# Kernel tuning notes

Hardware: AMD Instinct MI355X
Metric: run time of the kernel (lower is better)

## Reference

```python
import jax, jax.numpy as jnp
import numpy as np

N = 4096       # num nodes
E = 131072     # num edges (avg degree 32)
IN = 128       # in_channels
H = 256        # hidden_channels
NC = 16        # num_classes
NH = 4         # num_heads
HD = H // NH   # head dim
EPS = 1e-5


def setup_inputs() -> dict:
    key = jax.random.key(0)
    ks = jax.random.split(key, 16)
    p = lambda k, sh, s=0.05: jax.random.normal(k, sh, jnp.float32) * s
    return {
        "x": jax.random.normal(ks[0], (N, IN), jnp.float32),
        "edge_index": jax.random.randint(ks[1], (2, E), 0, N),
        "edge_attr": jax.random.uniform(ks[2], (E,), jnp.float32),
        # GCN layers
        "W_gcn1": p(ks[3], (IN, H)), "b_gcn1": jnp.zeros((H,), jnp.float32),
        "W_gcn2": p(ks[4], (H, H)), "b_gcn2": jnp.zeros((H,), jnp.float32),
        # Transformer encoder layer (post-norm, batch_first)
        "in_proj_w": p(ks[5], (3 * H, H)), "in_proj_b": jnp.zeros((3 * H,), jnp.float32),
        "out_proj_w": p(ks[6], (H, H)), "out_proj_b": jnp.zeros((H,), jnp.float32),
        "ln1_g": jnp.ones((H,), jnp.float32), "ln1_b": jnp.zeros((H,), jnp.float32),
        "ffn_w1": p(ks[7], (H, 4 * H)), "ffn_b1": jnp.zeros((4 * H,), jnp.float32),
        "ffn_w2": p(ks[8], (4 * H, H)), "ffn_b2": jnp.zeros((H,), jnp.float32),
        "ln2_g": jnp.ones((H,), jnp.float32), "ln2_b": jnp.zeros((H,), jnp.float32),
        # classifier head
        "W_cls": p(ks[9], (H, NC)), "b_cls": jnp.zeros((NC,), jnp.float32),
        # semantic decoder
        "W_d1": p(ks[10], (H, 2 * H)), "b_d1": jnp.zeros((2 * H,), jnp.float32),
        "W_d2": p(ks[11], (2 * H, 3)), "b_d2": jnp.zeros((3,), jnp.float32),
    }


def gcn_conv(x, edge_index, edge_weight, W, b):
    """PyG GCNConv: add self-loops, symmetric norm, gather-matmul-scatter."""
    n = x.shape[0]
    src, dst = edge_index[0], edge_index[1]
    loop = jnp.arange(n)
    src_f = jnp.concatenate([src, loop])
    dst_f = jnp.concatenate([dst, loop])
    ew_f = jnp.concatenate([edge_weight, jnp.ones((n,), x.dtype)])
    deg = jax.ops.segment_sum(ew_f, dst_f, num_segments=n)
    dinv = jnp.where(deg > 0, jax.lax.rsqrt(deg), 0.0)
    norm = dinv[src_f] * ew_f * dinv[dst_f]            # [E+N]
    h = x @ W                                          # [N,H]
    out = jax.ops.segment_sum(norm[:, None] * h[src_f], dst_f, num_segments=n)
    return out + b


def layer_norm(x, g, b):
    mu = jnp.mean(x, axis=-1, keepdims=True)
    var = jnp.mean(jnp.square(x - mu), axis=-1, keepdims=True)
    return (x - mu) * jax.lax.rsqrt(var + EPS) * g + b


def transformer_layer(x, in_proj_w, in_proj_b, out_proj_w, out_proj_b,
                      ln1_g, ln1_b, ffn_w1, ffn_b1, ffn_w2, ffn_b2, ln2_g, ln2_b):
    # Self-attention (seq = all N nodes, batch of 1), eval mode (no dropout)
    qkv = x @ in_proj_w.T + in_proj_b                  # [N,3H]
    q, k, v = jnp.split(qkv, 3, axis=-1)
    q = q.reshape(-1, NH, HD) * (1.0 / np.sqrt(HD))
    k = k.reshape(-1, NH, HD)
    v = v.reshape(-1, NH, HD)
    scores = jnp.einsum("nhd,mhd->hnm", q, k)          # [NH,N,N]
    attn = jax.nn.softmax(scores, axis=-1)
    ctx = jnp.einsum("hnm,mhd->nhd", attn, v).reshape(-1, H)
    attn_out = ctx @ out_proj_w.T + out_proj_b
    x = layer_norm(x + attn_out, ln1_g, ln1_b)         # post-norm
    ffn = jax.nn.relu(x @ ffn_w1 + ffn_b1) @ ffn_w2 + ffn_b2
    return layer_norm(x + ffn, ln2_g, ln2_b)


def reference(x, edge_index, edge_attr,
              W_gcn1, b_gcn1, W_gcn2, b_gcn2,
              in_proj_w, in_proj_b, out_proj_w, out_proj_b,
              ln1_g, ln1_b, ffn_w1, ffn_b1, ffn_w2, ffn_b2, ln2_g, ln2_b,
              W_cls, b_cls, W_d1, b_d1, W_d2, b_d2):
    x_local = jax.nn.relu(gcn_conv(x, edge_index, edge_attr, W_gcn1, b_gcn1))
    # F.dropout with training=False is identity
    x_local = gcn_conv(x_local, edge_index, edge_attr, W_gcn2, b_gcn2)
    x_global = transformer_layer(x_local, in_proj_w, in_proj_b, out_proj_w,
                                 out_proj_b, ln1_g, ln1_b, ffn_w1, ffn_b1,
                                 ffn_w2, ffn_b2, ln2_g, ln2_b)
    x_final = x_local + x_global
    out_cls = jax.nn.log_softmax(x_final @ W_cls + b_cls, axis=1)
    out_reco = jax.nn.sigmoid(jax.nn.relu(x_final @ W_d1 + b_d1) @ W_d2 + b_d2)
    return (out_cls, out_reco)
```

## Files before the change

### kernel.cpp

```cpp
#include <hip/hip_runtime.h>
#include <hip/hip_bf16.h>

#define N_NODES 4096
#define N_EDGES 131072
#define KSPLIT 8

typedef short bf16x8 __attribute__((ext_vector_type(8)));
typedef float f32x4  __attribute__((ext_vector_type(4)));

#if __has_builtin(__builtin_amdgcn_exp2f)
#define EXP2F __builtin_amdgcn_exp2f
#else
#define EXP2F exp2f
#endif

#define QSCL 0.1803368801111743f

static __device__ __forceinline__ float b2f(__hip_bfloat16 x) { return __bfloat162float(x); }
static __device__ __forceinline__ __hip_bfloat16 f2b(float x) { return __float2bfloat16(x); }
static __device__ __forceinline__ short f2bs(float x) {
    __hip_bfloat16 h = __float2bfloat16(x);
    return *reinterpret_cast<short*>(&h);
}
static __device__ __forceinline__ float us2f(ushort u) {
    union { unsigned i; float f; } x; x.i = ((unsigned)u) << 16; return x.f;
}
static __device__ __forceinline__ unsigned pack2(float lo, float hi) {
    return (unsigned)(ushort)f2bs(lo) | ((unsigned)(ushort)f2bs(hi) << 16);
}

static __device__ __forceinline__ float rmax16(float v) {
    v = fmaxf(v, __shfl_xor(v, 1));
    v = fmaxf(v, __shfl_xor(v, 2));
    v = fmaxf(v, __shfl_xor(v, 4));
    v = fmaxf(v, __shfl_xor(v, 8));
    return v;
}
static __device__ __forceinline__ float rsum16(float v) {
    v += __shfl_xor(v, 1);
    v += __shfl_xor(v, 2);
    v += __shfl_xor(v, 4);
    v += __shfl_xor(v, 8);
    return v;
}
static __device__ __forceinline__ int is_f32(const unsigned* ln1g_raw) {
    return ln1g_raw[0] == 0x3F800000u ? 1 : 0;
}
static __device__ __forceinline__ int is_i64(const unsigned* ei_raw) {
    unsigned acc = 0;
#pragma unroll
    for (int j = 1; j < 32; j += 2) acc |= ei_raw[j];
    return acc == 0u ? 1 : 0;
}

struct Ptrs24 { const void* p[24]; };

#define CAST_TOTAL 1681171

__global__ __launch_bounds__(256) void cast_all(Ptrs24 ptrs, const unsigned* __restrict__ ln1g_raw,
                                                __hip_bfloat16* __restrict__ canon,
                                                float* __restrict__ deg, int* __restrict__ cnt) {
    const int gi = blockIdx.x * 256 + threadIdx.x;
    if (gi < N_NODES) { deg[gi] = 1.0f; cnt[gi] = 0; }
    const int sizes[24] = {524288,131072,32768,256,65536,256,196608,768,65536,256,
                           256,256,262144,1024,262144,256,256,256,4096,16,
                           131072,512,1536,3};
    const long i0 = (long)gi * 8;
    if (i0 >= CAST_TOTAL) return;
    const int f32 = is_f32(ln1g_raw);
    int off = (int)i0, seg = 0, base = 0;
    bool done = false;
#pragma unroll
    for (int s = 0; s < 24; s++) {
        if (!done) {
            if (off < sizes[s]) { seg = s; done = true; }
            else { off -= sizes[s]; base += sizes[s]; }
        }
    }
    const void* p = ptrs.p[seg];
    ushort ov[8];
    int Rlog = -1, C = 0;
    if (seg == 2)       { Rlog = 7;  C = 256; }
    else if (seg == 4)  { Rlog = 8;  C = 256; }
    else if (seg == 12) { Rlog = 8;  C = 1024; }
    else if (seg == 14) { Rlog = 10; C = 256; }
    else if (seg == 20) { Rlog = 8;  C = 512; }
    if (Rlog >= 0) {
        const int c = off >> Rlog;
        const int k0 = off & ((1 << Rlog) - 1);
#pragma unroll
        for (int j = 0; j < 8; j++) {
            const int src = (k0 + j) * C + c;
            float v = f32 ? ((const float*)p)[src] : us2f(((const ushort*)p)[src]);
            ov[j] = (ushort)f2bs(v);
        }
    } else if (off + 8 > sizes[seg]) {
        for (int j = 0; j < 8; j++) {
            if (off + j < sizes[seg]) {
                float v = f32 ? ((const float*)p)[off + j] : us2f(((const ushort*)p)[off + j]);
                canon[base + off + j] = f2b(v);
            }
        }
        return;
    } else if (f32) {
        uint4 a = *(const uint4*)((const float*)p + off);
        uint4 b = *(const uint4*)((const float*)p + off + 4);
        const float* fa = (const float*)&a;
        const float* fb = (const float*)&b;
#pragma unroll
        for (int j = 0; j < 4; j++) { ov[j] = (ushort)f2bs(fa[j]); ov[4 + j] = (ushort)f2bs(fb[j]); }
    } else {
        uint4 a = *(const uint4*)((const ushort*)p + off);
        *(uint4*)ov = a;
    }
    *(uint4*)((ushort*)canon + base + off) = *(uint4*)ov;
}

static __device__ __forceinline__ int ld_idx(const void* ei, int k, int i64) {
    return i64 ? (int)((const long long*)ei)[k] : ((const int*)ei)[k];
}

__global__ __launch_bounds__(256) void deg_scat_k(const void* __restrict__ ei,
                                                  const __hip_bfloat16* __restrict__ ew,
                                                  float* deg, int* cnt) {
    const int i64 = is_i64((const unsigned*)ei);
    int e = blockIdx.x * 256 + threadIdx.x;
    if (e < N_EDGES) {
        int d = ld_idx(ei, N_EDGES + e, i64);
        atomicAdd(&deg[d], b2f(ew[e]));
        atomicAdd(&cnt[d], 1);
    }
}

__global__ __launch_bounds__(256) void scan_k(const float* __restrict__ deg, float* dinv,
                                              int* cnt, int* rowptr) {
    __shared__ int ss[256];
    const int t = threadIdx.x;
    const int base = t * 16;
    int loc[16];
    int run = 0;
#pragma unroll
    for (int j = 0; j < 16; j++) { loc[j] = run; run += cnt[base + j]; }
    ss[t] = run;
    __syncthreads();
    for (int off = 1; off < 256; off <<= 1) {
        int v = (t >= off) ? ss[t - off] : 0;
        __syncthreads();
        ss[t] += v;
        __syncthreads();
    }
    int pre = (t == 0) ? 0 : ss[t - 1];
#pragma unroll
    for (int j = 0; j < 16; j++) rowptr[base + j] = pre + loc[j];
    if (t == 255) rowptr[N_NODES] = pre + run;
    for (int i = t; i < N_NODES; i += 256) {
        float dg = deg[i];
        dinv[i] = dg > 0.f ? rsqrtf(dg) : 0.f;
        cnt[i] = 0;
    }
}

__global__ __launch_bounds__(256) void fill_k(const void* __restrict__ ei,
                                              const __hip_bfloat16* __restrict__ ew,
                                              const float* __restrict__ dinv,
                                              const int* __restrict__ rowptr,
                                              int* cur, int* csrc, float* cw) {
    const int i64 = is_i64((const unsigned*)ei);
    int e = blockIdx.x * 256 + threadIdx.x;
    if (e < N_EDGES) {
        int s = ld_idx(ei, e, i64), d = ld_idx(ei, N_EDGES + e, i64);
        int p = atomicAdd(&cur[d], 1);
        int slot = rowptr[d] + p;
        csrc[slot] = s;
        cw[slot] = dinv[s] * b2f(ew[e]) * dinv[d];
    }
}

template <bool RELU>
__global__ __launch_bounds__(256) void gcn_agg(const __hip_bfloat16* __restrict__ hf,
                                               const float* __restrict__ dinv,
                                               const int* __restrict__ rowptr,
                                               const int* __restrict__ csrc,
                                               const float* __restrict__ cw,
                                               const __hip_bfloat16* __restrict__ bias,
                                               __hip_bfloat16* __restrict__ out) {
    const int t = threadIdx.x;
    const int n = blockIdx.x * 4 + (t >> 6);
    const int c0 = (t & 63) * 4;
    const ushort* hp = (const ushort*)hf;
    const float di = dinv[n];
    float acc[4];
    {
        ushort4 own = *(const ushort4*)(hp + (size_t)n * 256 + c0);
        ushort4 bv  = *(const ushort4*)((const ushort*)bias + c0);
        const float dii = di * di;
        acc[0] = fmaf(dii, us2f(own.x), us2f(bv.x));
        acc[1] = fmaf(dii, us2f(own.y), us2f(bv.y));
        acc[2] = fmaf(dii, us2f(own.z), us2f(bv.z));
        acc[3] = fmaf(dii, us2f(own.w), us2f(bv.w));
    }
    int p = rowptr[n];
    const int end = rowptr[n + 1];
    for (; p + 4 <= end; p += 4) {
        int s0 = csrc[p], s1 = csrc[p + 1], s2 = csrc[p + 2], s3 = csrc[p + 3];
        float w0 = cw[p], w1 = cw[p + 1], w2 = cw[p + 2], w3 = cw[p + 3];
        ushort4 v0 = *(const ushort4*)(hp + (size_t)s0 * 256 + c0);
        ushort4 v1 = *(const ushort4*)(hp + (size_t)s1 * 256 + c0);
        ushort4 v2 = *(const ushort4*)(hp + (size_t)s2 * 256 + c0);
        ushort4 v3 = *(const ushort4*)(hp + (size_t)s3 * 256 + c0);
        acc[0] = fmaf(w0, us2f(v0.x), acc[0]); acc[1] = fmaf(w0, us2f(v0.y), acc[1]);
        acc[2] = fmaf(w0, us2f(v0.z), acc[2]); acc[3] = fmaf(w0, us2f(v0.w), acc[3]);
        acc[0] = fmaf(w1, us2f(v1.x), acc[0]); acc[1] = fmaf(w1, us2f(v1.y), acc[1]);
        acc[2] = fmaf(w1, us2f(v1.z), acc[2]); acc[3] = fmaf(w1, us2f(v1.w), acc[3]);
        acc[0] = fmaf(w2, us2f(v2.x), acc[0]); acc[1] = fmaf(w2, us2f(v2.y), acc[1]);
        acc[2] = fmaf(w2, us2f(v2.z), acc[2]); acc[3] = fmaf(w2, us2f(v2.w), acc[3]);
        acc[0] = fmaf(w3, us2f(v3.x), acc[0]); acc[1] = fmaf(w3, us2f(v3.y), acc[1]);
        acc[2] = fmaf(w3, us2f(v3.z), acc[2]); acc[3] = fmaf(w3, us2f(v3.w), acc[3]);
    }
    for (; p < end; p++) {
        int s = csrc[p];
        float wgt = cw[p];
        ushort4 v = *(const ushort4*)(hp + (size_t)s * 256 + c0);
        acc[0] = fmaf(wgt, us2f(v.x), acc[0]); acc[1] = fmaf(wgt, us2f(v.y), acc[1]);
        acc[2] = fmaf(wgt, us2f(v.z), acc[2]); acc[3] = fmaf(wgt, us2f(v.w), acc[3]);
    }
    if (RELU) {
#pragma unroll
        for (int j = 0; j < 4; j++) acc[j] = fmaxf(acc[j], 0.f);
    }
    ushort4 o;
    o.x = (ushort)f2bs(acc[0]); o.y = (ushort)f2bs(acc[1]);
    o.z = (ushort)f2bs(acc[2]); o.w = (ushort)f2bs(acc[3]);
    *(ushort4*)((ushort*)out + (size_t)n * 256 + c0) = o;
}

template <bool BIAS, bool RELU>
__global__ __launch_bounds__(256) void gemm64(const __hip_bfloat16* __restrict__ A,
                                              const __hip_bfloat16* __restrict__ Bt,
                                              const __hip_bfloat16* __restrict__ bias,
                                              __hip_bfloat16* __restrict__ C,
                                              int K, int Nn) {
    __shared__ __align__(16) short As[64 * 72];
    __shared__ __align__(16) short Bs[64 * 72];
    const int t = threadIdx.x;
    const int m0 = blockIdx.y * 64, n0 = blockIdx.x * 64;
    const int lane = t & 63, w = t >> 6, li = lane & 15, quad = lane >> 4;
    const int sr = t >> 3, sc = (t & 7) * 8;

    f32x4 acc[4];
#pragma unroll
    for (int i = 0; i < 4; i++) acc[i] = (f32x4){0.f, 0.f, 0.f, 0.f};

    uint4 pa[2], pb[2];
#pragma unroll
    for (int i = 0; i < 2; i++) {
        pa[i] = *(const uint4*)((const ushort*)A + (size_t)(m0 + i * 32 + sr) * K + sc);
        pb[i] = *(const uint4*)((const ushort*)Bt + (size_t)(n0 + i * 32 + sr) * K + sc);
    }

    const int NIT = K >> 6;
    for (int kb = 0; kb < NIT; kb++) {
#pragma unroll
        for (int i = 0; i < 2; i++) {
            *(uint4*)&As[(i * 32 + sr) * 72 + sc] = pa[i];
            *(uint4*)&Bs[(i * 32 + sr) * 72 + sc] = pb[i];
        }
        __syncthreads();
        if (kb + 1 < NIT) {
            const int kbase = (kb + 1) * 64;
#pragma unroll
            for (int i = 0; i < 2; i++) {
                pa[i] = *(const uint4*)((const ushort*)A + (size_t)(m0 + i * 32 + sr) * K + kbase + sc);
                pb[i] = *(const uint4*)((const ushort*)Bt + (size_t)(n0 + i * 32 + sr) * K + kbase + sc);
            }
        }
#pragma unroll
        for (int kk = 0; kk < 64; kk += 32) {
            bf16x8 a = *(const bf16x8*)&As[(w * 16 + li) * 72 + kk + quad * 8];
#pragma unroll
            for (int nt = 0; nt < 4; nt++) {
                bf16x8 b = *(const bf16x8*)&Bs[(nt * 16 + li) * 72 + kk + quad * 8];
                acc[nt] = __builtin_amdgcn_mfma_f32_16x16x32_bf16(a, b, acc[nt], 0, 0, 0);
            }
        }
        __syncthreads();
    }
#pragma unroll
    for (int nt = 0; nt < 4; nt++) {
        const int col = n0 + nt * 16 + li;
        const float bv = BIAS ? b2f(bias[col]) : 0.f;
#pragma unroll
        for (int r = 0; r < 4; r++) {
            const int row = m0 + w * 16 + quad * 4 + r;
            float v = acc[nt][r] + bv;
            if (RELU) v = fmaxf(v, 0.f);
            C[(size_t)row * Nn + col] = f2b(v);
        }
    }
}

template <bool BIAS, bool RELU>
__global__ __launch_bounds__(256) void gemm128(const __hip_bfloat16* __restrict__ A,
                                               const __hip_bfloat16* __restrict__ Bt,
                                               const __hip_bfloat16* __restrict__ bias,
                                               __hip_bfloat16* __restrict__ C,
                                               int K, int Nn) {
    __shared__ __align__(16) short As[128 * 72];
    __shared__ __align__(16) short Bs[128 * 72];
    const int t = threadIdx.x;
    const int m0 = blockIdx.y * 128, n0 = blockIdx.x * 128;
    const int lane = t & 63, w = t >> 6, li = lane & 15, quad = lane >> 4;
    const int wr = (w >> 1) * 64, wc = (w & 1) * 64;
    const int sr = t >> 3, sc = (t & 7) * 8;

    f32x4 acc[16];
#pragma unroll
    for (int i = 0; i < 16; i++) acc[i] = (f32x4){0.f, 0.f, 0.f, 0.f};

    uint4 pa[4], pb[4];
#pragma unroll
    for (int i = 0; i < 4; i++) {
        pa[i] = *(const uint4*)((const ushort*)A + (size_t)(m0 + i * 32 + sr) * K + sc);
        pb[i] = *(const uint4*)((const ushort*)Bt + (size_t)(n0 + i * 32 + sr) * K + sc);
    }

    const int NIT = K >> 6;
    for (int kb = 0; kb < NIT; kb++) {
#pragma unroll
        for (int i = 0; i < 4; i++) {
            *(uint4*)&As[(i * 32 + sr) * 72 + sc] = pa[i];
            *(uint4*)&Bs[(i * 32 + sr) * 72 + sc] = pb[i];
        }
        __syncthreads();
        if (kb + 1 < NIT) {
            const int kbase = (kb + 1) * 64;
#pragma unroll
            for (int i = 0; i < 4; i++) {
                pa[i] = *(const uint4*)((const ushort*)A + (size_t)(m0 + i * 32 + sr) * K + kbase + sc);
                pb[i] = *(const uint4*)((const ushort*)Bt + (size_t)(n0 + i * 32 + sr) * K + kbase + sc);
            }
        }
#pragma unroll
        for (int kk = 0; kk < 64; kk += 32) {
            bf16x8 a[4], b[4];
#pragma unroll
            for (int i = 0; i < 4; i++) {
                a[i] = *(const bf16x8*)&As[(wr + i * 16 + li) * 72 + kk + quad * 8];
                b[i] = *(const bf16x8*)&Bs[(wc + i * 16 + li) * 72 + kk + quad * 8];
            }
#pragma unroll
            for (int am = 0; am < 4; am++)
#pragma unroll
                for (int bn = 0; bn < 4; bn++)
                    acc[am * 4 + bn] = __builtin_amdgcn_mfma_f32_16x16x32_bf16(a[am], b[bn], acc[am * 4 + bn], 0, 0, 0);
        }
        __syncthreads();
    }
#pragma unroll
    for (int am = 0; am < 4; am++)
#pragma unroll
        for (int bn = 0; bn < 4; bn++) {
            const int col = n0 + wc + bn * 16 + li;
            const float bv = BIAS ? b2f(bias[col]) : 0.f;
#pragma unroll
            for (int r = 0; r < 4; r++) {
                const int row = m0 + wr + am * 16 + quad * 4 + r;
                float v = acc[am * 4 + bn][r] + bv;
                if (RELU) v = fmaxf(v, 0.f);
                C[(size_t)row * Nn + col] = f2b(v);
            }
        }
}

__global__ __launch_bounds__(256) void attn_part(const __hip_bfloat16* __restrict__ qkv,
                                                 __hip_bfloat16* __restrict__ Opart,
                                                 float* __restrict__ Lpart) {
    __shared__ __align__(16) short Ks[64 * 72];
    __shared__ __align__(16) short Vt[64 * 72];
    const int t = threadIdx.x;
    const int h = blockIdx.y;
    const int q0 = blockIdx.x * 64;
    const int kz = blockIdx.z;
    const int lane = t & 63, w = t >> 6, li = lane & 15, quad = lane >> 4;
    const ushort* qp = (const ushort*)qkv;

    const int kr0 = t >> 3, kd0 = (t & 7) * 8;
    const int jbeg = kz * (N_NODES / KSPLIT);
    const int jend = jbeg + N_NODES / KSPLIT;

    uint4 kreg0 = *(const uint4*)(qp + (size_t)(jbeg + kr0) * 768 + 256 + h * 64 + kd0);
    uint4 kreg1 = *(const uint4*)(qp + (size_t)(jbeg + 32 + kr0) * 768 + 256 + h * 64 + kd0);
    uint4 vreg0 = *(const uint4*)(qp + (size_t)(jbeg + lane) * 768 + 512 + h * 64 + w * 8);
    uint4 vreg1 = *(const uint4*)(qp + (size_t)(jbeg + lane) * 768 + 512 + h * 64 + (4 + w) * 8);

#pragma unroll
    for (int it = 0; it < 2; it++) {
        int idx = it * 256 + t;
        int r = idx >> 3, d = (idx & 7) * 8;
        uint4 v = *(const uint4*)(qp + (size_t)(q0 + r) * 768 + h * 64 + d);
        const ushort* sv = (const ushort*)&v;
        ushort ov[8];
#pragma unroll
        for (int j = 0; j < 8; j++) ov[j] = (ushort)f2bs(us2f(sv[j]) * QSCL);
        *(uint4*)&Ks[r * 72 + d] = *(uint4*)ov;
    }
    __syncthreads();
    bf16x8 qf0 = *(const bf16x8*)&Ks[(w * 16 + li) * 72 + 0  + quad * 8];
    bf16x8 qf1 = *(const bf16x8*)&Ks[(w * 16 + li) * 72 + 32 + quad * 8];
    __syncthreads();

    f32x4 O[4];
#pragma unroll
    for (int i = 0; i < 4; i++) O[i] = (f32x4){0.f, 0.f, 0.f, 0.f};
    float l_run = 0.f;

    const int srcA = 32 * (quad & 1) + li;
    const int srcB = srcA + 16;
    const int hi_t = (quad >> 1) & 1;

    for (int j0 = jbeg; j0 < jend; j0 += 64) {
        *(uint4*)&Ks[kr0 * 72 + kd0] = kreg0;
        *(uint4*)&Ks[(32 + kr0) * 72 + kd0] = kreg1;
        {
            const short* sv = (const short*)&vreg0;
#pragma unroll
            for (int j = 0; j < 8; j++) Vt[(w * 8 + j) * 72 + lane] = sv[j];
            const short* sw = (const short*)&vreg1;
#pragma unroll
            for (int j = 0; j < 8; j++) Vt[((4 + w) * 8 + j) * 72 + lane] = sw[j];
        }
        __syncthreads();
        if (j0 + 64 < jend) {
            kreg0 = *(const uint4*)(qp + (size_t)(j0 + 64 + kr0) * 768 + 256 + h * 64 + kd0);
            kreg1 = *(const uint4*)(qp + (size_t)(j0 + 96 + kr0) * 768 + 256 + h * 64 + kd0);
            vreg0 = *(const uint4*)(qp + (size_t)(j0 + 64 + lane) * 768 + 512 + h * 64 + w * 8);
            vreg1 = *(const uint4*)(qp + (size_t)(j0 + 64 + lane) * 768 + 512 + h * 64 + (4 + w) * 8);
        }

        f32x4 T[4];
#pragma unroll
        for (int i = 0; i < 4; i++) T[i] = (f32x4){0.f, 0.f, 0.f, 0.f};
#pragma unroll
        for (int nt = 0; nt < 4; nt++) {
            bf16x8 kf0 = *(const bf16x8*)&Ks[(nt * 16 + li) * 72 + 0  + quad * 8];
            bf16x8 kf1 = *(const bf16x8*)&Ks[(nt * 16 + li) * 72 + 32 + quad * 8];
            T[nt] = __builtin_amdgcn_mfma_f32_16x16x32_bf16(kf0, qf0, T[nt], 0, 0, 0);
            T[nt] = __builtin_amdgcn_mfma_f32_16x16x32_bf16(kf1, qf1, T[nt], 0, 0, 0);
        }

        float rs = 0.f;
#pragma unroll
        for (int nt = 0; nt < 4; nt++)
#pragma unroll
            for (int r = 0; r < 4; r++) {
                float p = EXP2F(T[nt][r]);
                T[nt][r] = p;
                rs += p;
            }
        rs += __shfl_xor(rs, 16);
        rs += __shfl_xor(rs, 32);
        l_run += rs;

        unsigned pd[4][2];
#pragma unroll
        for (int nt = 0; nt < 4; nt++) {
            pd[nt][0] = pack2(T[nt][0], T[nt][1]);
            pd[nt][1] = pack2(T[nt][2], T[nt][3]);
        }

#pragma unroll
        for (int c = 0; c < 2; c++) {
            const int tl = 2 * c, th = 2 * c + 1;
            unsigned aL0 = (unsigned)__shfl((int)pd[tl][0], srcA);
            unsigned aL1 = (unsigned)__shfl((int)pd[tl][1], srcA);
            unsigned aH0 = (unsigned)__shfl((int)pd[th][0], srcA);
            unsigned aH1 = (unsigned)__shfl((int)pd[th][1], srcA);
            unsigned bL0 = (unsigned)__shfl((int)pd[tl][0], srcB);
            unsigned bL1 = (unsigned)__shfl((int)pd[tl][1], srcB);
            unsigned bH0 = (unsigned)__shfl((int)pd[th][0], srcB);
            unsigned bH1 = (unsigned)__shfl((int)pd[th][1], srcB);
            unsigned af[4];
            af[0] = hi_t ? aH0 : aL0;
            af[1] = hi_t ? aH1 : aL1;
            af[2] = hi_t ? bH0 : bL0;
            af[3] = hi_t ? bH1 : bL1;
            bf16x8 afrag = *(const bf16x8*)af;
#pragma unroll
            for (int nt2 = 0; nt2 < 4; nt2++) {
                bf16x8 vf = *(const bf16x8*)&Vt[(nt2 * 16 + li) * 72 + c * 32 + quad * 8];
                O[nt2] = __builtin_amdgcn_mfma_f32_16x16x32_bf16(afrag, vf, O[nt2], 0, 0, 0);
            }
        }
        __syncthreads();
    }

    const int hb = kz * 4 + h;
    ushort* ob = (ushort*)Opart + ((size_t)hb * 4096 + q0) * 64;
#pragma unroll
    for (int nt = 0; nt < 4; nt++)
#pragma unroll
        for (int r = 0; r < 4; r++)
            ob[(size_t)(w * 16 + quad * 4 + r) * 64 + nt * 16 + li] = (ushort)f2bs(O[nt][r]);
    if (quad == 0)
        Lpart[(size_t)hb * 4096 + q0 + w * 16 + li] = l_run;
}

__global__ __launch_bounds__(256) void attn_comb(const __hip_bfloat16* __restrict__ Opart,
                                                 const float* __restrict__ Lpart,
                                                 __hip_bfloat16* __restrict__ ctx) {
    const int t = threadIdx.x;
    const int h = blockIdx.y;
    const int row = blockIdx.x * 64 + (t >> 2);
    const int d0 = (t & 3) * 16;
    float L = 0.f;
#pragma unroll
    for (int s = 0; s < KSPLIT; s++) L += Lpart[(size_t)(s * 4 + h) * 4096 + row];
    const float inv = 1.f / L;
    float o[16];
#pragma unroll
    for (int j = 0; j < 16; j++) o[j] = 0.f;
#pragma unroll
    for (int s = 0; s < KSPLIT; s++) {
        const ushort* base = (const ushort*)Opart + ((size_t)(s * 4 + h) * 4096 + row) * 64 + d0;
        uint4 v0 = *(const uint4*)base;
        uint4 v1 = *(const uint4*)(base + 8);
        const ushort* sv0 = (const ushort*)&v0;
        const ushort* sv1 = (const ushort*)&v1;
#pragma unroll
        for (int j = 0; j < 8; j++) {
            o[j]     += us2f(sv0[j]);
            o[8 + j] += us2f(sv1[j]);
        }
    }
    ushort pk[16];
#pragma unroll
    for (int j = 0; j < 16; j++) pk[j] = (ushort)f2bs(o[j] * inv);
    ushort* dst = (ushort*)ctx + (size_t)row * 256 + h * 64 + d0;
    *(uint4*)dst = *(uint4*)pk;
    *(uint4*)(dst + 8) = *(uint4*)(pk + 8);
}

template <bool ADDC>
__global__ __launch_bounds__(256) void ln256(const __hip_bfloat16* __restrict__ A,
                                             const __hip_bfloat16* __restrict__ Bv,
                                             const __hip_bfloat16* __restrict__ gw,
                                             const __hip_bfloat16* __restrict__ bw,
                                             const __hip_bfloat16* __restrict__ Cadd,
                                             __hip_bfloat16* __restrict__ out) {
    __shared__ float red[8];
    const int row = blockIdx.x, c = threadIdx.x;
    const size_t o = (size_t)row * 256 + c;
    float x = b2f(A[o]) + b2f(Bv[o]);
    float s = x;
#pragma unroll
    for (int m = 1; m < 64; m <<= 1) s += __shfl_xor(s, m);
    const int wv = c >> 6;
    if ((c & 63) == 0) red[wv] = s;
    __syncthreads();
    float mu = (red[0] + red[1] + red[2] + red[3]) * (1.f / 256.f);
    float d = x - mu;
    float s2 = d * d;
#pragma unroll
    for (int m = 1; m < 64; m <<= 1) s2 += __shfl_xor(s2, m);
    if ((c & 63) == 0) red[4 + wv] = s2;
    __syncthreads();
    float var = (red[4] + red[5] + red[6] + red[7]) * (1.f / 256.f);
    float y = d * rsqrtf(var + 1e-5f) * b2f(gw[c]) + b2f(bw[c]);
    if (ADDC) y += b2f(Cadd[o]);
    out[o] = f2b(y);
}

__global__ __launch_bounds__(256) void cls_reco(const __hip_bfloat16* __restrict__ xf,
                                                const __hip_bfloat16* __restrict__ Wcls,
                                                const __hip_bfloat16* __restrict__ bcls,
                                                const __hip_bfloat16* __restrict__ Wd1t,
                                                const __hip_bfloat16* __restrict__ bd1,
                                                const __hip_bfloat16* __restrict__ Wd2,
                                                const __hip_bfloat16* __restrict__ bd2,
                                                const unsigned* __restrict__ ln1g_raw,
                                                void* __restrict__ out) {
    __shared__ __align__(16) char smem[49408];
    const int t = threadIdx.x;
    if (blockIdx.x < 256) {
        float* Ws = (float*)smem;
        float* bs = (float*)(smem + 16384);
        for (int i = t; i < 4096; i += 256) Ws[i] = b2f(Wcls[i]);
        if (t < 16) bs[t] = b2f(bcls[t]);
        __syncthreads();
        const int c = t & 15, rl = t >> 4;
        const int row = blockIdx.x * 16 + rl;
        const ushort* xr = (const ushort*)xf + (size_t)row * 256;
        float acc = bs[c];
        for (int k0 = 0; k0 < 256; k0 += 8) {
            uint4 v = *(const uint4*)(xr + k0);
            const ushort* sv = (const ushort*)&v;
#pragma unroll
            for (int j = 0; j < 8; j++) acc = fmaf(us2f(sv[j]), Ws[(k0 + j) * 16 + c], acc);
        }
        float mx = rmax16(acc);
        float se = rsum16(__expf(acc - mx));
        float v = acc - mx - __logf(se);
        const size_t oidx = (size_t)row * 16 + c;
        if (is_f32(ln1g_raw)) ((float*)out)[oidx] = v;
        else                  ((__hip_bfloat16*)out)[oidx] = f2b(v);
    } else {
        short* As = (short*)smem;
        short* Bs = (short*)(smem + 1280);
        float* W2s = (float*)(smem + 42240);
        float (*red)[16][3] = (float (*)[16][3])(smem + 48384);
        const int m0 = (blockIdx.x - 256) * 16;
        const int lane = t & 63, w = t >> 6, li = lane & 15, quad = lane >> 4;
        const ushort* Ap = (const ushort*)xf;
        const ushort* Bp = (const ushort*)Wd1t;
        const int K = 256;

        for (int i = t; i < 1536; i += 256) W2s[i] = b2f(Wd2[i]);

        f32x4 acc[8];
#pragma unroll
        for (int i = 0; i < 8; i++) acc[i] = (f32x4){0.f, 0.f, 0.f, 0.f};

        const int bn = t >> 2, bk0 = (t & 3) * 8;
        const int ar = t >> 2, ak0 = (t & 3) * 8;

        uint4 breg[8];
        uint4 areg;
#pragma unroll
        for (int it2 = 0; it2 < 8; it2++)
            breg[it2] = *(const uint4*)(Bp + (size_t)(it2 * 64 + bn) * K + bk0);
        if (t < 64) areg = *(const uint4*)(Ap + (size_t)(m0 + ar) * K + ak0);

        for (int kb = 0; kb < 8; kb++) {
#pragma unroll
            for (int it2 = 0; it2 < 8; it2++)
                *(uint4*)&Bs[(it2 * 64 + bn) * 40 + bk0] = breg[it2];
            if (t < 64) *(uint4*)&As[ar * 40 + ak0] = areg;
            __syncthreads();
            if (kb + 1 < 8) {
                const int kbase = (kb + 1) * 32;
#pragma unroll
                for (int it2 = 0; it2 < 8; it2++)
                    breg[it2] = *(const uint4*)(Bp + (size_t)(it2 * 64 + bn) * K + kbase + bk0);
                if (t < 64) areg = *(const uint4*)(Ap + (size_t)(m0 + ar) * K + kbase + ak0);
            }
            bf16x8 a = *(const bf16x8*)&As[li * 40 + quad * 8];
#pragma unroll
            for (int nt = 0; nt < 8; nt++) {
                bf16x8 b = *(const bf16x8*)&Bs[(w * 128 + nt * 16 + li) * 40 + quad * 8];
                acc[nt] = __builtin_amdgcn_mfma_f32_16x16x32_bf16(a, b, acc[nt], 0, 0, 0);
            }
            __syncthreads();
        }

        float p3[3][4];
#pragma unroll
        for (int c = 0; c < 3; c++)
#pragma unroll
            for (int r = 0; r < 4; r++) p3[c][r] = 0.f;
#pragma unroll
        for (int nt = 0; nt < 8; nt++) {
            const int col = w * 128 + nt * 16 + li;
            const float bv = b2f(bd1[col]);
            const float w0 = W2s[col * 3 + 0], w1 = W2s[col * 3 + 1], w2 = W2s[col * 3 + 2];
#pragma unroll
            for (int r = 0; r < 4; r++) {
                float hv = fmaxf(acc[nt][r] + bv, 0.f);
                p3[0][r] = fmaf(hv, w0, p3[0][r]);
                p3[1][r] = fmaf(hv, w1, p3[1][r]);
                p3[2][r] = fmaf(hv, w2, p3[2][r]);
            }
        }
#pragma unroll
        for (int c = 0; c < 3; c++)
#pragma unroll
            for (int r = 0; r < 4; r++) {
                float s = rsum16(p3[c][r]);
                if (li == 0) red[w][quad * 4 + r][c] = s;
            }
        __syncthreads();
        if (t < 48) {
            const int rl = t / 3, c = t % 3;
            float s = red[0][rl][c] + red[1][rl][c] + red[2][rl][c] + red[3][rl][c] + b2f(bd2[c]);
            float v = 1.f / (1.f + __expf(-s));
            const size_t oidx = (size_t)(N_NODES * 16) + (size_t)(m0 + rl) * 3 + c;
            if (is_f32(ln1g_raw)) ((float*)out)[oidx] = v;
            else                  ((__hip_bfloat16*)out)[oidx] = f2b(v);
        }
    }
}

extern "C" void kernel_launch(void* const* d_in, const int* in_sizes, int n_in,
                              void* d_out, int out_size, void* d_ws, size_t ws_size,
                              hipStream_t stream) {
    char* ws = (char*)d_ws;
    __hip_bfloat16* canon = (__hip_bfloat16*)(ws + 256);
    float* deg    = (float*)(ws + 3362816);
    int*   cnt    = (int*)  (ws + 3379200);
    int*   rowptr = (int*)  (ws + 3395584);
    float* dinv   = (float*)(ws + 3412224);
    int*   csrc   = (int*)  (ws + 3428608);
    float* cw     = (float*)(ws + 3952896);
    __hip_bfloat16* h     = (__hip_bfloat16*)(ws + 4477184);
    __hip_bfloat16* x1    = (__hip_bfloat16*)(ws + 6574336);
    __hip_bfloat16* xloc  = (__hip_bfloat16*)(ws + 8671488);
    __hip_bfloat16* big   = (__hip_bfloat16*)(ws + 10768640);
    __hip_bfloat16* ctxp  = (__hip_bfloat16*)(ws + 19157248);
    __hip_bfloat16* attno = (__hip_bfloat16*)(ws + 21254400);
    __hip_bfloat16* y1    = (__hip_bfloat16*)(ws + 23351552);
    __hip_bfloat16* xfin  = (__hip_bfloat16*)(ws + 25448704);
    __hip_bfloat16* Opart = (__hip_bfloat16*)(ws + 27545856);
    float* Lpart = (float*)(ws + 6574336);

    const __hip_bfloat16* xc    = canon + 0;
    const __hip_bfloat16* eac   = canon + 524288;
    const __hip_bfloat16* Wg1   = canon + 655360;
    const __hip_bfloat16* bg1   = canon + 688128;
    const __hip_bfloat16* Wg2   = canon + 688384;
    const __hip_bfloat16* bg2   = canon + 753920;
    const __hip_bfloat16* ipw   = canon + 754176;
    const __hip_bfloat16* ipb   = canon + 950784;
    const __hip_bfloat16* opw   = canon + 951552;
    const __hip_bfloat16* opb   = canon + 1017088;
    const __hip_bfloat16* ln1g  = canon + 1017344;
    const __hip_bfloat16* ln1b  = canon + 1017600;
    const __hip_bfloat16* fw1   = canon + 1017856;
    const __hip_bfloat16* fb1   = canon + 1280000;
    const __hip_bfloat16* fw2   = canon + 1281024;
    const __hip_bfloat16* fb2   = canon + 1543168;
    const __hip_bfloat16* ln2g  = canon + 1543424;
    const __hip_bfloat16* ln2b  = canon + 1543680;
    const __hip_bfloat16* Wcls  = canon + 1543936;
    const __hip_bfloat16* bcls  = canon + 1548032;
    const __hip_bfloat16* Wd1   = canon + 1548048;
    const __hip_bfloat16* bd1   = canon + 1679120;
    const __hip_bfloat16* Wd2   = canon + 1679632;
    const __hip_bfloat16* bd2   = canon + 1681168;

    const void* ei = d_in[1];
    const unsigned* ln1g_raw = (const unsigned*)d_in[11];

    Ptrs24 pt;
    {
        const int map[24] = {0,2,3,4,5,6,7,8,9,10,11,12,13,14,15,16,17,18,19,20,21,22,23,24};
        for (int i = 0; i < 24; i++) pt.p[i] = d_in[map[i]];
    }

    const dim3 b256(256);

    cast_all<<<(CAST_TOTAL / 8 + 256) / 256, b256, 0, stream>>>(pt, ln1g_raw, canon, deg, cnt);

    deg_scat_k<<<512, b256, 0, stream>>>(ei, eac, deg, cnt);
    scan_k<<<1, b256, 0, stream>>>(deg, dinv, cnt, rowptr);
    fill_k<<<512, b256, 0, stream>>>(ei, eac, dinv, rowptr, cnt, csrc, cw);

    gemm64<false, false><<<dim3(4, 64), b256, 0, stream>>>(xc, Wg1, nullptr, h, 128, 256);
    gcn_agg<true><<<1024, b256, 0, stream>>>(h, dinv, rowptr, csrc, cw, bg1, x1);
    gemm64<false, false><<<dim3(4, 64), b256, 0, stream>>>(x1, Wg2, nullptr, h, 256, 256);
    gcn_agg<false><<<1024, b256, 0, stream>>>(h, dinv, rowptr, csrc, cw, bg2, xloc);

    gemm128<true, false><<<dim3(6, 32), b256, 0, stream>>>(xloc, ipw, ipb, big, 256, 768);
    attn_part<<<dim3(64, 4, KSPLIT), b256, 0, stream>>>(big, Opart, Lpart);
    attn_comb<<<dim3(64, 4), b256, 0, stream>>>(Opart, Lpart, ctxp);
    gemm64<true, false><<<dim3(4, 64), b256, 0, stream>>>(ctxp, opw, opb, attno, 256, 256);
    ln256<false><<<4096, b256, 0, stream>>>(xloc, attno, ln1g, ln1b, nullptr, y1);
    gemm128<true, true><<<dim3(8, 32), b256, 0, stream>>>(y1, fw1, fb1, big, 256, 1024);
    gemm64<true, false><<<dim3(4, 64), b256, 0, stream>>>(big, fw2, fb2, ctxp, 1024, 256);
    ln256<true><<<4096, b256, 0, stream>>>(y1, ctxp, ln2g, ln2b, xloc, xfin);

    cls_reco<<<512, b256, 0, stream>>>(xfin, Wcls, bcls, Wd1, bd1, Wd2, bd2, ln1g_raw, d_out);
}
```

Before: 330.4 us.

## Fuse attention combine, out-proj and LayerNorm; pre-transpose V in QKV epilogue

The QKV GEMM epilogue now writes the V slice transposed into a separate buffer. The attention kernel can then load V tiles with vector stores instead of scattered per-element LDS writes. A new row-block GEMM kernel merges the split-K attention partials and applies the output projection, bias, residual and LayerNorm in one pass. The same kernel handles the FFN down-projection with its LayerNorm and the final residual add. This removes four launches and several intermediate round trips through global memory, but the fused GEMM runs only 64 blocks, each owning a full 256-column row tile, so parallelism drops sharply, especially for the K=1024 FFN GEMM.

```diff
diff --git a/kernel.cpp b/kernel.cpp
--- a/kernel.cpp
+++ b/kernel.cpp
@@ -299,11 +299,12 @@
     }
 }
 
-template <bool BIAS, bool RELU>
+template <bool BIAS, bool RELU, bool VT>
 __global__ __launch_bounds__(256) void gemm128(const __hip_bfloat16* __restrict__ A,
                                                const __hip_bfloat16* __restrict__ Bt,
                                                const __hip_bfloat16* __restrict__ bias,
                                                __hip_bfloat16* __restrict__ C,
+                                               ushort* __restrict__ vtg,
                                                int K, int Nn) {
     __shared__ __align__(16) short As[128 * 72];
     __shared__ __align__(16) short Bs[128 * 72];
@@ -360,19 +361,31 @@
     for (int am = 0; am < 4; am++)
 #pragma unroll
         for (int bn = 0; bn < 4; bn++) {
-            const int col = n0 + wc + bn * 16 + li;
+            const int c0 = n0 + wc + bn * 16;
+            const int col = c0 + li;
             const float bv = BIAS ? b2f(bias[col]) : 0.f;
-#pragma unroll
-            for (int r = 0; r < 4; r++) {
-                const int row = m0 + wr + am * 16 + quad * 4 + r;
-                float v = acc[am * 4 + bn][r] + bv;
-                if (RELU) v = fmaxf(v, 0.f);
-                C[(size_t)row * Nn + col] = f2b(v);
+            if (VT && c0 >= 512) {
+                const int r0 = m0 + wr + am * 16 + quad * 4;
+                ushort4 o;
+                o.x = (ushort)f2bs(acc[am * 4 + bn][0] + bv);
+                o.y = (ushort)f2bs(acc[am * 4 + bn][1] + bv);
+                o.z = (ushort)f2bs(acc[am * 4 + bn][2] + bv);
+                o.w = (ushort)f2bs(acc[am * 4 + bn][3] + bv);
+                *(ushort4*)(vtg + (size_t)(col - 512) * 4096 + r0) = o;
+            } else {
+#pragma unroll
+                for (int r = 0; r < 4; r++) {
+                    const int row = m0 + wr + am * 16 + quad * 4 + r;
+                    float v = acc[am * 4 + bn][r] + bv;
+                    if (RELU) v = fmaxf(v, 0.f);
+                    C[(size_t)row * Nn + col] = f2b(v);
+                }
             }
         }
 }
 
 __global__ __launch_bounds__(256) void attn_part(const __hip_bfloat16* __restrict__ qkv,
+                                                 const ushort* __restrict__ vtg,
                                                  __hip_bfloat16* __restrict__ Opart,
                                                  float* __restrict__ Lpart) {
     __shared__ __align__(16) short Ks[64 * 72];
@@ -390,8 +403,8 @@
 
     uint4 kreg0 = *(const uint4*)(qp + (size_t)(jbeg + kr0) * 768 + 256 + h * 64 + kd0);
     uint4 kreg1 = *(const uint4*)(qp + (size_t)(jbeg + 32 + kr0) * 768 + 256 + h * 64 + kd0);
-    uint4 vreg0 = *(const uint4*)(qp + (size_t)(jbeg + lane) * 768 + 512 + h * 64 + w * 8);
-    uint4 vreg1 = *(const uint4*)(qp + (size_t)(jbeg + lane) * 768 + 512 + h * 64 + (4 + w) * 8);
+    uint4 vreg0 = *(const uint4*)(vtg + (size_t)(h * 64 + kr0) * 4096 + jbeg + kd0);
+    uint4 vreg1 = *(const uint4*)(vtg + (size_t)(h * 64 + 32 + kr0) * 4096 + jbeg + kd0);
 
 #pragma unroll
     for (int it = 0; it < 2; it++) {
@@ -421,20 +434,14 @@
     for (int j0 = jbeg; j0 < jend; j0 += 64) {
         *(uint4*)&Ks[kr0 * 72 + kd0] = kreg0;
         *(uint4*)&Ks[(32 + kr0) * 72 + kd0] = kreg1;
-        {
-            const short* sv = (const short*)&vreg0;
-#pragma unroll
-            for (int j = 0; j < 8; j++) Vt[(w * 8 + j) * 72 + lane] = sv[j];
-            const short* sw = (const short*)&vreg1;
-#pragma unroll
-            for (int j = 0; j < 8; j++) Vt[((4 + w) * 8 + j) * 72 + lane] = sw[j];
-        }
+        *(uint4*)&Vt[kr0 * 72 + kd0] = vreg0;
+        *(uint4*)&Vt[(32 + kr0) * 72 + kd0] = vreg1;
         __syncthreads();
         if (j0 + 64 < jend) {
             kreg0 = *(const uint4*)(qp + (size_t)(j0 + 64 + kr0) * 768 + 256 + h * 64 + kd0);
             kreg1 = *(const uint4*)(qp + (size_t)(j0 + 96 + kr0) * 768 + 256 + h * 64 + kd0);
-            vreg0 = *(const uint4*)(qp + (size_t)(j0 + 64 + lane) * 768 + 512 + h * 64 + w * 8);
-            vreg1 = *(const uint4*)(qp + (size_t)(j0 + 64 + lane) * 768 + 512 + h * 64 + (4 + w) * 8);
+            vreg0 = *(const uint4*)(vtg + (size_t)(h * 64 + kr0) * 4096 + j0 + 64 + kd0);
+            vreg1 = *(const uint4*)(vtg + (size_t)(h * 64 + 32 + kr0) * 4096 + j0 + 64 + kd0);
         }
 
         f32x4 T[4];
@@ -505,69 +512,136 @@
         Lpart[(size_t)hb * 4096 + q0 + w * 16 + li] = l_run;
 }
 
-__global__ __launch_bounds__(256) void attn_comb(const __hip_bfloat16* __restrict__ Opart,
-                                                 const float* __restrict__ Lpart,
-                                                 __hip_bfloat16* __restrict__ ctx) {
+template <bool COMB, bool ADDAFTER>
+__global__ __launch_bounds__(256) void gemm_rowln(const __hip_bfloat16* __restrict__ Asrc,
+                                                  const float* __restrict__ Lpart,
+                                                  const __hip_bfloat16* __restrict__ Bt,
+                                                  const __hip_bfloat16* __restrict__ bias,
+                                                  const __hip_bfloat16* __restrict__ res,
+                                                  const __hip_bfloat16* __restrict__ gw,
+                                                  const __hip_bfloat16* __restrict__ bw,
+                                                  const __hip_bfloat16* __restrict__ addsrc,
+                                                  __hip_bfloat16* __restrict__ out, int K) {
+    __shared__ __align__(16) short As[64 * 72];
+    __shared__ __align__(16) short Bs[256 * 72];
     const int t = threadIdx.x;
-    const int h = blockIdx.y;
-    const int row = blockIdx.x * 64 + (t >> 2);
-    const int d0 = (t & 3) * 16;
-    float L = 0.f;
-#pragma unroll
-    for (int s = 0; s < KSPLIT; s++) L += Lpart[(size_t)(s * 4 + h) * 4096 + row];
-    const float inv = 1.f / L;
-    float o[16];
-#pragma unroll
-    for (int j = 0; j < 16; j++) o[j] = 0.f;
-#pragma unroll
-    for (int s = 0; s < KSPLIT; s++) {
-        const ushort* base = (const ushort*)Opart + ((size_t)(s * 4 + h) * 4096 + row) * 64 + d0;
-        uint4 v0 = *(const uint4*)base;
-        uint4 v1 = *(const uint4*)(base + 8);
-        const ushort* sv0 = (const ushort*)&v0;
-        const ushort* sv1 = (const ushort*)&v1;
-#pragma unroll
-        for (int j = 0; j < 8; j++) {
-            o[j]     += us2f(sv0[j]);
-            o[8 + j] += us2f(sv1[j]);
-        }
-    }
-    ushort pk[16];
-#pragma unroll
-    for (int j = 0; j < 16; j++) pk[j] = (ushort)f2bs(o[j] * inv);
-    ushort* dst = (ushort*)ctx + (size_t)row * 256 + h * 64 + d0;
-    *(uint4*)dst = *(uint4*)pk;
-    *(uint4*)(dst + 8) = *(uint4*)(pk + 8);
-}
-
-template <bool ADDC>
-__global__ __launch_bounds__(256) void ln256(const __hip_bfloat16* __restrict__ A,
-                                             const __hip_bfloat16* __restrict__ Bv,
-                                             const __hip_bfloat16* __restrict__ gw,
-                                             const __hip_bfloat16* __restrict__ bw,
-                                             const __hip_bfloat16* __restrict__ Cadd,
-                                             __hip_bfloat16* __restrict__ out) {
-    __shared__ float red[8];
-    const int row = blockIdx.x, c = threadIdx.x;
-    const size_t o = (size_t)row * 256 + c;
-    float x = b2f(A[o]) + b2f(Bv[o]);
-    float s = x;
-#pragma unroll
-    for (int m = 1; m < 64; m <<= 1) s += __shfl_xor(s, m);
-    const int wv = c >> 6;
-    if ((c & 63) == 0) red[wv] = s;
-    __syncthreads();
-    float mu = (red[0] + red[1] + red[2] + red[3]) * (1.f / 256.f);
-    float d = x - mu;
-    float s2 = d * d;
-#pragma unroll
-    for (int m = 1; m < 64; m <<= 1) s2 += __shfl_xor(s2, m);
-    if ((c & 63) == 0) red[4 + wv] = s2;
-    __syncthreads();
-    float var = (red[4] + red[5] + red[6] + red[7]) * (1.f / 256.f);
-    float y = d * rsqrtf(var + 1e-5f) * b2f(gw[c]) + b2f(bw[c]);
-    if (ADDC) y += b2f(Cadd[o]);
-    out[o] = f2b(y);
+    const int m0 = blockIdx.x * 64;
+    const int lane = t & 63, w = t >> 6, li = lane & 15, quad = lane >> 4;
+    const ushort* Ap = (const ushort*)Asrc;
+    const ushort* Bp = (const ushort*)Bt;
+    const int NIT = K >> 6;
+
+    f32x4 acc[16];
+#pragma unroll
+    for (int i = 0; i < 16; i++) acc[i] = (f32x4){0.f, 0.f, 0.f, 0.f};
+
+    const int bn = t >> 3, bk0 = (t & 7) * 8;
+    const int ar = t >> 2, ak0 = (t & 3) * 16;
+
+    uint4 breg[8];
+    uint4 areg[2];
+#pragma unroll
+    for (int it2 = 0; it2 < 8; it2++)
+        breg[it2] = *(const uint4*)(Bp + (size_t)(it2 * 32 + bn) * K + bk0);
+    if (!COMB) {
+        areg[0] = *(const uint4*)(Ap + (size_t)(m0 + ar) * K + ak0);
+        areg[1] = *(const uint4*)(Ap + (size_t)(m0 + ar) * K + ak0 + 8);
+    }
+
+    for (int kb = 0; kb < NIT; kb++) {
+#pragma unroll
+        for (int it2 = 0; it2 < 8; it2++)
+            *(uint4*)&Bs[(it2 * 32 + bn) * 72 + bk0] = breg[it2];
+        if (COMB) {
+            const int hd = kb;
+            const int gr = m0 + ar;
+            float L = 0.f;
+#pragma unroll
+            for (int s = 0; s < KSPLIT; s++) L += Lpart[(size_t)(s * 4 + hd) * 4096 + gr];
+            const float inv = 1.f / L;
+            float sum[16];
+#pragma unroll
+            for (int j = 0; j < 16; j++) sum[j] = 0.f;
+#pragma unroll
+            for (int s = 0; s < KSPLIT; s++) {
+                const ushort* ob = Ap + ((size_t)(s * 4 + hd) * 4096 + gr) * 64 + ak0;
+                uint4 v0 = *(const uint4*)ob;
+                uint4 v1 = *(const uint4*)(ob + 8);
+                const ushort* s0 = (const ushort*)&v0;
+                const ushort* s1 = (const ushort*)&v1;
+#pragma unroll
+                for (int j = 0; j < 8; j++) { sum[j] += us2f(s0[j]); sum[8 + j] += us2f(s1[j]); }
+            }
+            ushort ov[16];
+#pragma unroll
+            for (int j = 0; j < 16; j++) ov[j] = (ushort)f2bs(sum[j] * inv);
+            *(uint4*)&As[ar * 72 + ak0] = *(uint4*)ov;
+            *(uint4*)&As[ar * 72 + ak0 + 8] = *(uint4*)(ov + 8);
+        } else {
+            *(uint4*)&As[ar * 72 + ak0] = areg[0];
+            *(uint4*)&As[ar * 72 + ak0 + 8] = areg[1];
+        }
+        __syncthreads();
+        if (kb + 1 < NIT) {
+            const int kbase = (kb + 1) * 64;
+#pragma unroll
+            for (int it2 = 0; it2 < 8; it2++)
+                breg[it2] = *(const uint4*)(Bp + (size_t)(it2 * 32 + bn) * K + kbase + bk0);
+            if (!COMB) {
+                areg[0] = *(const uint4*)(Ap + (size_t)(m0 + ar) * K + kbase + ak0);
+                areg[1] = *(const uint4*)(Ap + (size_t)(m0 + ar) * K + kbase + ak0 + 8);
+            }
+        }
+#pragma unroll
+        for (int kk = 0; kk < 64; kk += 32) {
+            bf16x8 a = *(const bf16x8*)&As[(w * 16 + li) * 72 + kk + quad * 8];
+#pragma unroll
+            for (int nt = 0; nt < 16; nt++) {
+                bf16x8 b = *(const bf16x8*)&Bs[(nt * 16 + li) * 72 + kk + quad * 8];
+                acc[nt] = __builtin_amdgcn_mfma_f32_16x16x32_bf16(a, b, acc[nt], 0, 0, 0);
+            }
+        }
+        __syncthreads();
+    }
+
+    float sx[4], sq[4];
+#pragma unroll
+    for (int r = 0; r < 4; r++) { sx[r] = 0.f; sq[r] = 0.f; }
+#pragma unroll
+    for (int nt = 0; nt < 16; nt++) {
+        const int col = nt * 16 + li;
+        const float bv = b2f(bias[col]);
+#pragma unroll
+        for (int r = 0; r < 4; r++) {
+            const int row = m0 + w * 16 + quad * 4 + r;
+            float v = acc[nt][r] + bv + b2f(res[(size_t)row * 256 + col]);
+            acc[nt][r] = v;
+            sx[r] += v;
+            sq[r] += v * v;
+        }
+    }
+    float mu[4], rstd[4];
+#pragma unroll
+    for (int r = 0; r < 4; r++) {
+        float S = rsum16(sx[r]);
+        float Q = rsum16(sq[r]);
+        float m = S * (1.f / 256.f);
+        float var = Q * (1.f / 256.f) - m * m;
+        mu[r] = m;
+        rstd[r] = rsqrtf(var + 1e-5f);
+    }
+#pragma unroll
+    for (int nt = 0; nt < 16; nt++) {
+        const int col = nt * 16 + li;
+        const float gv = b2f(gw[col]), bv2 = b2f(bw[col]);
+#pragma unroll
+        for (int r = 0; r < 4; r++) {
+            const int row = m0 + w * 16 + quad * 4 + r;
+            float y = (acc[nt][r] - mu[r]) * rstd[r] * gv + bv2;
+            if (ADDAFTER) y += b2f(addsrc[(size_t)row * 256 + col]);
+            out[(size_t)row * 256 + col] = f2b(y);
+        }
+    }
 }
 
 __global__ __launch_bounds__(256) void cls_reco(const __hip_bfloat16* __restrict__ xf,
@@ -704,8 +778,7 @@
     __hip_bfloat16* x1    = (__hip_bfloat16*)(ws + 6574336);
     __hip_bfloat16* xloc  = (__hip_bfloat16*)(ws + 8671488);
     __hip_bfloat16* big   = (__hip_bfloat16*)(ws + 10768640);
-    __hip_bfloat16* ctxp  = (__hip_bfloat16*)(ws + 19157248);
-    __hip_bfloat16* attno = (__hip_bfloat16*)(ws + 21254400);
+    ushort*         vtg   = (ushort*)(ws + 21254400);
     __hip_bfloat16* y1    = (__hip_bfloat16*)(ws + 23351552);
     __hip_bfloat16* xfin  = (__hip_bfloat16*)(ws + 25448704);
     __hip_bfloat16* Opart = (__hip_bfloat16*)(ws + 27545856);
@@ -758,14 +831,13 @@
     gemm64<false, false><<<dim3(4, 64), b256, 0, stream>>>(x1, Wg2, nullptr, h, 256, 256);
     gcn_agg<false><<<1024, b256, 0, stream>>>(h, dinv, rowptr, csrc, cw, bg2, xloc);
 
-    gemm128<true, false><<<dim3(6, 32), b256, 0, stream>>>(xloc, ipw, ipb, big, 256, 768);
-    attn_part<<<dim3(64, 4, KSPLIT), b256, 0, stream>>>(big, Opart, Lpart);
-    attn_comb<<<dim3(64, 4), b256, 0, stream>>>(Opart, Lpart, ctxp);
-    gemm64<true, false><<<dim3(4, 64), b256, 0, stream>>>(ctxp, opw, opb, attno, 256, 256);
-    ln256<false><<<4096, b256, 0, stream>>>(xloc, attno, ln1g, ln1b, nullptr, y1);
-    gemm128<true, true><<<dim3(8, 32), b256, 0, stream>>>(y1, fw1, fb1, big, 256, 1024);
-    gemm64<true, false><<<dim3(4, 64), b256, 0, stream>>>(big, fw2, fb2, ctxp, 1024, 256);
-    ln256<true><<<4096, b256, 0, stream>>>(y1, ctxp, ln2g, ln2b, xloc, xfin);
+    gemm128<true, false, true><<<dim3(6, 32), b256, 0, stream>>>(xloc, ipw, ipb, big, vtg, 256, 768);
+    attn_part<<<dim3(64, 4, KSPLIT), b256, 0, stream>>>(big, vtg, Opart, Lpart);
+    gemm_rowln<true, false><<<64, b256, 0, stream>>>((const __hip_bfloat16*)Opart, Lpart, opw, opb,
+                                                     xloc, ln1g, ln1b, nullptr, y1, 256);
+    gemm128<true, true, false><<<dim3(8, 32), b256, 0, stream>>>(y1, fw1, fb1, big, nullptr, 256, 1024);
+    gemm_rowln<false, true><<<64, b256, 0, stream>>>(big, nullptr, fw2, fb2, y1, ln2g, ln2b,
+                                                     xloc, xfin, 1024);
 
     cls_reco<<<512, b256, 0, stream>>>(xfin, Wcls, bcls, Wd1, bd1, Wd2, bd2, ln1g_raw, d_out);
 }
```

Result: slower. 378.3 us (+14.5%).
